# Optimization experiments

Hardware: AMD Instinct MI355X
Metric: run time of the kernel (lower is better)

Reference implementation:

```python
import jax, jax.numpy as jnp
import numpy as np


def setup_inputs() -> dict:
    key = jax.random.key(0)
    k1, k2 = jax.random.split(key)
    B, N, D = 4, 4096, 512
    q = jax.random.normal(k1, (B, N, D), dtype=jnp.float32)
    kv = jax.random.normal(k2, (B, N, D), dtype=jnp.float32)
    return {"q": q, "kv": kv}


def reference(q, kv):
    # q, kv: [B, N, D]
    scale = (kv.shape[-1] // 2) ** (-0.5)
    # full QK^T needed for the softmax row normalizer: [B, N, N]
    scores = jnp.einsum('bnd,bmd->bnm', q, kv) * scale
    lse = jax.nn.logsumexp(scores, axis=-1)          # [B, N]
    # diagonal logits computed directly (avoids re-reading the full matrix)
    diag = jnp.einsum('bnd,bnd->bn', q, kv) * scale  # [B, N]
    # masked_select with an eye mask returns the diagonal softmax entries,
    # flattened in row-major order -> shape [B*N]
    return jnp.exp(diag - lse).reshape(-1)
```

## Files before the change

### kernel.cpp

```cpp
#include <hip/hip_runtime.h>
#include <hip/hip_fp16.h>


typedef _Float16 f16x8 __attribute__((ext_vector_type(8)));
typedef float    f32x4 __attribute__((ext_vector_type(4)));

#define NB 4
#define NN 4096
#define ND 512
#define SCALE 0.0625f
#define NROWS (NB * NN)
#define TROWS 32
#define RPITCH 1040
#define TBYTES (TROWS * RPITCH)

__device__ __forceinline__ void gld16(const void* g, void* l) {
    __builtin_amdgcn_global_load_lds(
        (const __attribute__((address_space(1))) unsigned int*)g,
        (__attribute__((address_space(3))) unsigned int*)l, 16, 0, 0);
}

__device__ __forceinline__ f16x8 cvt8(float4 a, float4 b) {
    f16x8 r;
    r[0] = (_Float16)a.x; r[1] = (_Float16)a.y; r[2] = (_Float16)a.z; r[3] = (_Float16)a.w;
    r[4] = (_Float16)b.x; r[5] = (_Float16)b.y; r[6] = (_Float16)b.z; r[7] = (_Float16)b.w;
    return r;
}

__launch_bounds__(256)
__global__ void convert_kernel(const float* __restrict__ q,
                               const float* __restrict__ kv,
                               _Float16* __restrict__ kvh,
                               float* __restrict__ diag) {
    const int row  = blockIdx.x * 4 + (threadIdx.x >> 6);
    const int lane = threadIdx.x & 63;

    const float4* kr = (const float4*)(kv + (size_t)row * ND) + lane * 2;
    const float4* qr = (const float4*)(q  + (size_t)row * ND) + lane * 2;
    float4 k0 = kr[0], k1 = kr[1];
    float4 q0 = qr[0], q1 = qr[1];

    *(f16x8*)(kvh + (size_t)row * ND + lane * 8) = cvt8(k0, k1);

    float dot = q0.x * k0.x;
    dot = fmaf(q0.y, k0.y, dot); dot = fmaf(q0.z, k0.z, dot); dot = fmaf(q0.w, k0.w, dot);
    dot = fmaf(q1.x, k1.x, dot); dot = fmaf(q1.y, k1.y, dot);
    dot = fmaf(q1.z, k1.z, dot); dot = fmaf(q1.w, k1.w, dot);

    dot += __shfl_xor(dot, 1, 64);
    dot += __shfl_xor(dot, 2, 64);
    dot += __shfl_xor(dot, 4, 64);
    dot += __shfl_xor(dot, 8, 64);
    dot += __shfl_xor(dot, 16, 64);
    dot += __shfl_xor(dot, 32, 64);
    if (lane == 0) diag[row] = dot;
}

__launch_bounds__(256, 2)
__global__ void lse_partial_kernel(const float* __restrict__ q,
                                   const _Float16* __restrict__ kvh,
                                   float* __restrict__ partial) {
    __shared__ char sbuf[2][TBYTES];

    const int bc = blockIdx.x;
    const int b  = bc >> 2;
    const int cs = bc & 3;
    const int rb = blockIdx.y;
    const int tid  = threadIdx.x;
    const int wid  = tid >> 6;
    const int lane = tid & 63;
    const int l15  = lane & 15;
    const int quad = lane >> 4;

    const int row0 = rb * 128 + wid * 32;

    f16x8 Af[2][16];
    #pragma unroll
    for (int m = 0; m < 2; ++m) {
        const float* qrow = q + ((size_t)(b * NN + row0 + m * 16 + l15)) * ND + quad * 8;
        #pragma unroll
        for (int k = 0; k < 16; ++k) {
            float4 u0 = *(const float4*)(qrow + k * 32);
            float4 u1 = *(const float4*)(qrow + k * 32 + 4);
            Af[m][k] = cvt8(u0, u1);
        }
    }

    float lacc[2][4];
    #pragma unroll
    for (int m = 0; m < 2; ++m)
        #pragma unroll
        for (int j = 0; j < 4; ++j)
            lacc[m][j] = 0.f;

    unsigned base_nf[2];
    #pragma unroll
    for (int nf = 0; nf < 2; ++nf)
        base_nf[nf] = (unsigned)((nf * 16 + l15) * RPITCH + quad * 16);

    const _Float16* kvbase = kvh + ((size_t)(b * NN + cs * 1024)) * ND;

    #define STAGE(it_, buf_)                                                 \
        do {                                                                 \
            const _Float16* gb_ = kvbase + (size_t)(it_) * TROWS * ND;       \
            char* lb_ = sbuf[buf_];                                          \
            _Pragma("unroll")                                                \
            for (int p_ = 0; p_ < 8; ++p_) {                                 \
                int r_ = wid * 8 + p_;                                       \
                gld16(gb_ + (size_t)r_ * ND + lane * 8, lb_ + r_ * RPITCH);  \
            }                                                                \
        } while (0)

    STAGE(0, 0);
    int buf = 0;

    for (int it = 0; it < 32; ++it) {
        __syncthreads();
        if (it + 1 < 32) STAGE(it + 1, buf ^ 1);

        const char* lb = sbuf[buf];
        f32x4 acc[2][2];
        #pragma unroll
        for (int m = 0; m < 2; ++m)
            #pragma unroll
            for (int nf = 0; nf < 2; ++nf)
                acc[m][nf] = (f32x4){0.f, 0.f, 0.f, 0.f};

        #pragma unroll
        for (int kt = 0; kt < 16; ++kt) {
            f16x8 bf[2];
            #pragma unroll
            for (int nf = 0; nf < 2; ++nf)
                bf[nf] = *(const f16x8*)(lb + base_nf[nf] + kt * 64);
            #pragma unroll
            for (int nf = 0; nf < 2; ++nf)
                #pragma unroll
                for (int m = 0; m < 2; ++m)
                    acc[m][nf] = __builtin_amdgcn_mfma_f32_16x16x32_f16(
                        Af[m][kt], bf[nf], acc[m][nf], 0, 0, 0);
        }

        #pragma unroll
        for (int m = 0; m < 2; ++m)
            #pragma unroll
            for (int nf = 0; nf < 2; ++nf)
                #pragma unroll
                for (int j = 0; j < 4; ++j)
                    lacc[m][j] += __expf(acc[m][nf][j] * SCALE);

        buf ^= 1;
    }

    #pragma unroll
    for (int m = 0; m < 2; ++m)
        #pragma unroll
        for (int j = 0; j < 4; ++j) {
            float v = lacc[m][j];
            v += __shfl_xor(v, 1, 64);
            v += __shfl_xor(v, 2, 64);
            v += __shfl_xor(v, 4, 64);
            v += __shfl_xor(v, 8, 64);
            if (l15 == 0)
                partial[(size_t)cs * NROWS + b * NN + row0 + m * 16 + quad * 4 + j] = v;
        }
}

__launch_bounds__(256)
__global__ void finalize_kernel(const float* __restrict__ partial,
                                const float* __restrict__ diag,
                                float* __restrict__ out) {
    const int idx = blockIdx.x * 256 + threadIdx.x;
    float l = partial[idx] + partial[NROWS + idx] +
              partial[2 * NROWS + idx] + partial[3 * NROWS + idx];
    out[idx] = __expf(diag[idx] * SCALE) / l;
}

extern "C" void kernel_launch(void* const* d_in, const int* in_sizes, int n_in,
                              void* d_out, int out_size, void* d_ws, size_t ws_size,
                              hipStream_t stream) {
    const float* q  = (const float*)d_in[0];
    const float* kv = (const float*)d_in[1];
    float* out = (float*)d_out;

    _Float16* kvh   = (_Float16*)d_ws;
    float* partial  = (float*)((char*)d_ws + (size_t)NROWS * ND * 2);
    float* diag     = partial + 4 * NROWS;

    convert_kernel<<<NROWS / 4, 256, 0, stream>>>(q, kv, kvh, diag);
    lse_partial_kernel<<<dim3(16, 32), 256, 0, stream>>>(q, kvh, partial);
    finalize_kernel<<<NROWS / 256, 256, 0, stream>>>(partial, diag, out);
}
```

Before: 168.4 us.

## Load half of each KV tile directly into registers instead of LDS

Each 32-row KV tile is now split in two. The first 16 rows are still staged through LDS with async global-to-LDS loads. The second 16 rows are read by every wave straight from global memory into 16 register fragments. This halves the LDS buffer and the LDS read traffic, which may raise occupancy or relieve LDS bandwidth. In exchange it adds redundant global or L2 reads across the 4 waves, a lot of register pressure from the extra 16 f16x8 fragments, and exposed global-load latency inside the loop.

```diff
diff --git a/kernel.cpp b/kernel.cpp
--- a/kernel.cpp
+++ b/kernel.cpp
@@ -10,9 +10,8 @@
 #define ND 512
 #define SCALE 0.0625f
 #define NROWS (NB * NN)
-#define TROWS 32
 #define RPITCH 1040
-#define TBYTES (TROWS * RPITCH)
+#define TBYTES (16 * RPITCH)
 
 __device__ __forceinline__ void gld16(const void* g, void* l) {
     __builtin_amdgcn_global_load_lds(
@@ -93,20 +92,18 @@
         for (int j = 0; j < 4; ++j)
             lacc[m][j] = 0.f;
 
-    unsigned base_nf[2];
-    #pragma unroll
-    for (int nf = 0; nf < 2; ++nf)
-        base_nf[nf] = (unsigned)((nf * 16 + l15) * RPITCH + quad * 16);
+    const unsigned base0 = (unsigned)(l15 * RPITCH + quad * 16);
 
     const _Float16* kvbase = kvh + ((size_t)(b * NN + cs * 1024)) * ND;
+    const _Float16* g1base = kvbase + (size_t)(16 + l15) * ND + quad * 8;
 
     #define STAGE(it_, buf_)                                                 \
         do {                                                                 \
-            const _Float16* gb_ = kvbase + (size_t)(it_) * TROWS * ND;       \
+            const _Float16* gb_ = kvbase + (size_t)(it_) * 32 * ND;          \
             char* lb_ = sbuf[buf_];                                          \
             _Pragma("unroll")                                                \
-            for (int p_ = 0; p_ < 8; ++p_) {                                 \
-                int r_ = wid * 8 + p_;                                       \
+            for (int p_ = 0; p_ < 4; ++p_) {                                 \
+                int r_ = wid * 4 + p_;                                       \
                 gld16(gb_ + (size_t)r_ * ND + lane * 8, lb_ + r_ * RPITCH);  \
             }                                                                \
         } while (0)
@@ -116,6 +113,15 @@
 
     for (int it = 0; it < 32; ++it) {
         __syncthreads();
+
+        f16x8 bn[16];
+        {
+            const _Float16* g1 = g1base + (size_t)it * 32 * ND;
+            #pragma unroll
+            for (int kt = 0; kt < 16; ++kt)
+                bn[kt] = *(const f16x8*)(g1 + kt * 32);
+        }
+
         if (it + 1 < 32) STAGE(it + 1, buf ^ 1);
 
         const char* lb = sbuf[buf];
@@ -128,16 +134,14 @@
 
         #pragma unroll
         for (int kt = 0; kt < 16; ++kt) {
-            f16x8 bf[2];
-            #pragma unroll
-            for (int nf = 0; nf < 2; ++nf)
-                bf[nf] = *(const f16x8*)(lb + base_nf[nf] + kt * 64);
-            #pragma unroll
-            for (int nf = 0; nf < 2; ++nf)
-                #pragma unroll
-                for (int m = 0; m < 2; ++m)
-                    acc[m][nf] = __builtin_amdgcn_mfma_f32_16x16x32_f16(
-                        Af[m][kt], bf[nf], acc[m][nf], 0, 0, 0);
+            f16x8 b0 = *(const f16x8*)(lb + base0 + kt * 64);
+            acc[0][0] = __builtin_amdgcn_mfma_f32_16x16x32_f16(Af[0][kt], b0, acc[0][0], 0, 0, 0);
+            acc[1][0] = __builtin_amdgcn_mfma_f32_16x16x32_f16(Af[1][kt], b0, acc[1][0], 0, 0, 0);
+        }
+        #pragma unroll
+        for (int kt = 0; kt < 16; ++kt) {
+            acc[0][1] = __builtin_amdgcn_mfma_f32_16x16x32_f16(Af[0][kt], bn[kt], acc[0][1], 0, 0, 0);
+            acc[1][1] = __builtin_amdgcn_mfma_f32_16x16x32_f16(Af[1][kt], bn[kt], acc[1][1], 0, 0, 0);
         }
 
         #pragma unroll
```

Result: slower. 240.4 us (+42.7%).
